# Kernel tuning notes

Measured on AMD Instinct MI355X. Metric: run time of the kernel, lower is better.

## Reference

```python
import jax, jax.numpy as jnp
import numpy as np

LARGE_NUMBER = 1e10
HIDDEN = 256
G = 32
NV = 64


def setup_inputs() -> dict:
    key = jax.random.key(0)
    k1, k2, k3, k4, k5, k6 = jax.random.split(key, 6)
    z = jax.random.normal(k1, (G * NV, HIDDEN), dtype=jnp.float32)
    mask = jax.random.randint(k2, (G * NV, 1), 0, 2).astype(jnp.float32)
    s = 1.0 / np.sqrt(HIDDEN)
    Wc = jax.random.uniform(k3, (HIDDEN, HIDDEN), jnp.float32, -s, s)
    bc = jax.random.uniform(k4, (HIDDEN,), jnp.float32, -s, s)
    Wy = jax.random.uniform(k5, (HIDDEN, HIDDEN), jnp.float32, -s, s)
    by = jax.random.uniform(k6, (HIDDEN,), jnp.float32, -s, s)
    return {"num_graphs": G, "nv": NV, "z": z, "mask": mask,
            "Wc": Wc, "bc": bc, "Wy": Wy, "by": by}


def reference(num_graphs, nv, z, mask, Wc, bc, Wy, by):
    H = z.shape[-1]
    z = z.reshape(num_graphs, nv, H)
    m = mask.reshape(num_graphs, nv, -1)          # [G, nv, 1]
    # Project ONCE per node (linearity makes this identical to projecting the
    # tiled [G,nv,nv,H] tensors as the torch code does).
    c = jnp.einsum('gnh,oh->gno', z, Wc) + bc     # lin_attention_c(z)
    y = jnp.einsum('gnh,oh->gno', z, Wy) + by     # lin_attention_y(z)
    # mask term: (m_i*L - L) + (m_j*L - L)
    mask_term = (m[:, :, None, :] + m[:, None, :, :]) * LARGE_NUMBER - 2.0 * LARGE_NUMBER
    # pairwise broadcast add + sigmoid: [G, nv, nv, H]
    s = jax.nn.sigmoid(c[:, :, None, :] + y[:, None, :, :] + mask_term)
    denom = jnp.sum(m, axis=1)[:, None, :]        # [G, 1, 1]
    out = jnp.sum(s, axis=2) / denom              # [G, nv, H]
    return out.reshape(-1, H)
```

## Files before the change

kernel.cpp:

```cpp
#include <hip/hip_runtime.h>

#define Gn    32
#define NVn   64
#define Hn    256
#define NROWS (Gn * NVn)

typedef __attribute__((ext_vector_type(8))) short  bf16x8;
typedef __attribute__((ext_vector_type(4))) float  f32x4;

__device__ inline unsigned short f2bf(float f) {
    unsigned int u = __builtin_bit_cast(unsigned int, f);
    return (unsigned short)((u + 0x7FFFu + ((u >> 16) & 1u)) >> 16);
}

__global__ __launch_bounds__(512) void gemm_exp_mfma(
    const float* __restrict__ z,
    const float* __restrict__ Wc, const float* __restrict__ bc,
    const float* __restrict__ Wy, const float* __restrict__ by,
    float* __restrict__ ws)
{
    const int n0    = blockIdx.x * 64;
    const int o0    = blockIdx.y * 64;
    const int which = blockIdx.z;
    const float* __restrict__ W    = which ? Wy : Wc;
    const float* __restrict__ bias = which ? by : bc;
    float* __restrict__ dst = ws + (size_t)which * NROWS * Hn;

    __shared__ unsigned short Za[64][40];
    __shared__ unsigned short Wb[64][40];

    const int t    = threadIdx.x;
    const int half = t >> 8;
    const int tt   = t & 255;
    const int srow = tt >> 2;
    const int sk   = (tt & 3) * 8;

    const float* src = half ? (W + (size_t)(o0 + srow) * Hn + sk)
                            : (z + (size_t)(n0 + srow) * Hn + sk);
    unsigned short* ldst = half ? &Wb[srow][sk] : &Za[srow][sk];

    const int wv = t >> 6;
    const int l  = t & 63;
    const int lm = l & 15;
    const int lq = l >> 4;
    const int ns = (wv & 3) * 16;
    const int oh = (wv >> 2) * 32;

    f32x4 acc[2] = {{0.f,0.f,0.f,0.f},{0.f,0.f,0.f,0.f}};

    float4 p0 = *(const float4*)(src);
    float4 p1 = *(const float4*)(src + 4);

    for (int kk = 0; kk < 8; ++kk) {
        bf16x8 v;
        v[0] = (short)f2bf(p0.x); v[1] = (short)f2bf(p0.y);
        v[2] = (short)f2bf(p0.z); v[3] = (short)f2bf(p0.w);
        v[4] = (short)f2bf(p1.x); v[5] = (short)f2bf(p1.y);
        v[6] = (short)f2bf(p1.z); v[7] = (short)f2bf(p1.w);
        *(bf16x8*)ldst = v;
        __syncthreads();

        if (kk < 7) {
            p0 = *(const float4*)(src + (kk + 1) * 32);
            p1 = *(const float4*)(src + (kk + 1) * 32 + 4);
        }

        const bf16x8 af = *(const bf16x8*)&Za[ns + lm][lq * 8];
        const bf16x8 b0 = *(const bf16x8*)&Wb[oh + lm][lq * 8];
        const bf16x8 b1 = *(const bf16x8*)&Wb[oh + 16 + lm][lq * 8];
        acc[0] = __builtin_amdgcn_mfma_f32_16x16x32_bf16(af, b0, acc[0], 0, 0, 0);
        acc[1] = __builtin_amdgcn_mfma_f32_16x16x32_bf16(af, b1, acc[1], 0, 0, 0);
        __syncthreads();
    }

#pragma unroll
    for (int ot = 0; ot < 2; ++ot) {
        const int o  = o0 + oh + ot * 16 + lm;
        const float bv = bias[o];
#pragma unroll
        for (int r = 0; r < 4; ++r) {
            const int n = n0 + ns + lq * 4 + r;
            dst[(size_t)n * Hn + o] = __expf(-(acc[ot][r] + bv));
        }
    }
}

__global__ __launch_bounds__(512) void pair_kernel(
    const float* __restrict__ mask,
    const float* __restrict__ ws,
    float* __restrict__ out)
{
    const float* __restrict__ ec = ws;
    const float* __restrict__ ey = ws + (size_t)NROWS * Hn;

    const int g  = blockIdx.x >> 3;
    const int i0 = (blockIdx.x & 7) * 8;
    const int t  = threadIdx.x;
    const int i  = i0 + (t >> 6);
    const int oc = (t & 63) * 4;

    __shared__ int act[64];
    __shared__ int cnt_s;

    if (t < 64) {
        const float m = mask[g * NVn + t];
        const unsigned long long b = __ballot(m != 0.f);
        const int below = __popcll(b & ((1ull << t) - 1ull));
        if (m != 0.f) act[below] = t;
        if (t == 0) cnt_s = (int)__popcll(b);
    }
    __syncthreads();
    const int cnt = cnt_s;

    const int row_i = g * NVn + i;
    float* po = out + (size_t)row_i * Hn + oc;

    const float mi = mask[row_i];
    if (mi == 0.f) {
        float4 zr; zr.x = zr.y = zr.z = zr.w = 0.f;
        *(float4*)po = zr;
        return;
    }

    const float4 ec4 = *(const float4*)(ec + (size_t)row_i * Hn + oc);
    const float* eyg = ey + (size_t)g * NVn * Hn + oc;

    float ax = 0.f, ay = 0.f, az = 0.f, aw = 0.f;
#pragma unroll 4
    for (int jj = 0; jj < cnt; ++jj) {
        const int j = act[jj];
        const float4 e4 = *(const float4*)(eyg + (size_t)j * Hn);
        ax += __builtin_amdgcn_rcpf(__builtin_fmaf(ec4.x, e4.x, 1.f));
        ay += __builtin_amdgcn_rcpf(__builtin_fmaf(ec4.y, e4.y, 1.f));
        az += __builtin_amdgcn_rcpf(__builtin_fmaf(ec4.z, e4.z, 1.f));
        aw += __builtin_amdgcn_rcpf(__builtin_fmaf(ec4.w, e4.w, 1.f));
    }

    const float s = 1.f / (float)cnt;
    float4 o4;
    o4.x = ax * s; o4.y = ay * s; o4.z = az * s; o4.w = aw * s;
    *(float4*)po = o4;
}

extern "C" void kernel_launch(void* const* d_in, const int* in_sizes, int n_in,
                              void* d_out, int out_size, void* d_ws, size_t ws_size,
                              hipStream_t stream) {
    const float* z    = (const float*)d_in[2];
    const float* mask = (const float*)d_in[3];
    const float* Wc   = (const float*)d_in[4];
    const float* bc   = (const float*)d_in[5];
    const float* Wy   = (const float*)d_in[6];
    const float* by   = (const float*)d_in[7];
    float* out = (float*)d_out;
    float* ws  = (float*)d_ws;

    dim3 gridA(NROWS / 64, Hn / 64, 2);
    gemm_exp_mfma<<<gridA, 512, 0, stream>>>(z, Wc, bc, Wy, by, ws);

    pair_kernel<<<Gn * 8, 512, 0, stream>>>(mask, ws, out);
}
```

Measured before the change: 81.33 us.

## Fuse projection GEMM and pairwise sigmoid sum into one per-graph kernel

The two kernels (MFMA projection with exp, then pairwise reduction) become a single kernel. Each block handles one graph and a 32-wide output slice, projects it with both weight matrices, and keeps the exp(-y) tile in shared memory for the pairwise sum. This removes the round trip of both projections through global memory and one kernel launch. In exchange, each block reloads and converts the whole 64x256 z tile for its graph, eight times per graph in total, and uses more shared memory per block. Block IDs are also remapped so blocks of the same graph are spread out.

```diff
diff --git a/kernel.cpp b/kernel.cpp
--- a/kernel.cpp
+++ b/kernel.cpp
@@ -3,7 +3,9 @@
 #define Gn    32
 #define NVn   64
 #define Hn    256
-#define NROWS (Gn * NVn)
+#define OT    32
+#define ZPAD  264
+#define EPAD  34
 
 typedef __attribute__((ext_vector_type(8))) short  bf16x8;
 typedef __attribute__((ext_vector_type(4))) float  f32x4;
@@ -13,133 +15,125 @@
     return (unsigned short)((u + 0x7FFFu + ((u >> 16) & 1u)) >> 16);
 }
 
-__global__ __launch_bounds__(512) void gemm_exp_mfma(
-    const float* __restrict__ z,
+__global__ __launch_bounds__(512) void fused_attn(
+    const float* __restrict__ z,  const float* __restrict__ mask,
     const float* __restrict__ Wc, const float* __restrict__ bc,
     const float* __restrict__ Wy, const float* __restrict__ by,
-    float* __restrict__ ws)
+    float* __restrict__ out)
 {
-    const int n0    = blockIdx.x * 64;
-    const int o0    = blockIdx.y * 64;
-    const int which = blockIdx.z;
-    const float* __restrict__ W    = which ? Wy : Wc;
-    const float* __restrict__ bias = which ? by : bc;
-    float* __restrict__ dst = ws + (size_t)which * NROWS * Hn;
+    const int phys = blockIdx.x;
+    const int lid  = (phys & 7) * 32 + (phys >> 3);
+    const int g    = lid >> 3;
+    const int o0   = (lid & 7) * OT;
 
-    __shared__ unsigned short Za[64][40];
-    __shared__ unsigned short Wb[64][40];
+    __shared__ __align__(16) unsigned short Zs[NVn][ZPAD];
+    __shared__ __align__(16) unsigned short Wsh[2 * OT][ZPAD];
+    __shared__ float eyL[NVn][EPAD];
+    __shared__ float mskL[NVn];
+    __shared__ int   act[NVn];
+    __shared__ int   cnt_s;
 
-    const int t    = threadIdx.x;
-    const int half = t >> 8;
-    const int tt   = t & 255;
-    const int srow = tt >> 2;
-    const int sk   = (tt & 3) * 8;
+    const int t = threadIdx.x;
 
-    const float* src = half ? (W + (size_t)(o0 + srow) * Hn + sk)
-                            : (z + (size_t)(n0 + srow) * Hn + sk);
-    unsigned short* ldst = half ? &Wb[srow][sk] : &Za[srow][sk];
+    if (t < 64) {
+        const float m = mask[g * NVn + t];
+        mskL[t] = m;
+        const unsigned long long b = __ballot(m != 0.f);
+        const int below = __popcll(b & ((1ull << t) - 1ull));
+        if (m != 0.f) act[below] = t;
+        if (t == 0) cnt_s = (int)__popcll(b);
+    }
+
+    const float* zg = z + (size_t)g * NVn * Hn;
+    float4 za[4], zb[4], wa[4], wb[4];
+#pragma unroll
+    for (int c = 0; c < 4; ++c) {
+        const int idx = t + c * 512;
+        const int row = idx >> 5;
+        const int k8  = (idx & 31) * 8;
+        const float* s = zg + (size_t)row * Hn + k8;
+        za[c] = *(const float4*)(s);
+        zb[c] = *(const float4*)(s + 4);
+    }
+#pragma unroll
+    for (int c = 0; c < 4; ++c) {
+        const int idx = t + c * 512;
+        const int row = idx >> 5;
+        const int k8  = (idx & 31) * 8;
+        const float* s = (row < OT) ? (Wc + (size_t)(o0 + row) * Hn + k8)
+                                    : (Wy + (size_t)(o0 + row - OT) * Hn + k8);
+        wa[c] = *(const float4*)(s);
+        wb[c] = *(const float4*)(s + 4);
+    }
+#pragma unroll
+    for (int c = 0; c < 4; ++c) {
+        const int idx = t + c * 512;
+        const int row = idx >> 5;
+        const int k8  = (idx & 31) * 8;
+        bf16x8 v;
+        v[0] = (short)f2bf(za[c].x); v[1] = (short)f2bf(za[c].y);
+        v[2] = (short)f2bf(za[c].z); v[3] = (short)f2bf(za[c].w);
+        v[4] = (short)f2bf(zb[c].x); v[5] = (short)f2bf(zb[c].y);
+        v[6] = (short)f2bf(zb[c].z); v[7] = (short)f2bf(zb[c].w);
+        *(bf16x8*)&Zs[row][k8] = v;
+        bf16x8 w;
+        w[0] = (short)f2bf(wa[c].x); w[1] = (short)f2bf(wa[c].y);
+        w[2] = (short)f2bf(wa[c].z); w[3] = (short)f2bf(wa[c].w);
+        w[4] = (short)f2bf(wb[c].x); w[5] = (short)f2bf(wb[c].y);
+        w[6] = (short)f2bf(wb[c].z); w[7] = (short)f2bf(wb[c].w);
+        *(bf16x8*)&Wsh[row][k8] = w;
+    }
+    __syncthreads();
 
     const int wv = t >> 6;
     const int l  = t & 63;
     const int lm = l & 15;
     const int lq = l >> 4;
     const int ns = (wv & 3) * 16;
-    const int oh = (wv >> 2) * 32;
+    const int oh = (wv >> 2) * 16;
 
-    f32x4 acc[2] = {{0.f,0.f,0.f,0.f},{0.f,0.f,0.f,0.f}};
-
-    float4 p0 = *(const float4*)(src);
-    float4 p1 = *(const float4*)(src + 4);
-
+    f32x4 accC = {0.f, 0.f, 0.f, 0.f};
+    f32x4 accY = {0.f, 0.f, 0.f, 0.f};
+#pragma unroll
     for (int kk = 0; kk < 8; ++kk) {
-        bf16x8 v;
-        v[0] = (short)f2bf(p0.x); v[1] = (short)f2bf(p0.y);
-        v[2] = (short)f2bf(p0.z); v[3] = (short)f2bf(p0.w);
-        v[4] = (short)f2bf(p1.x); v[5] = (short)f2bf(p1.y);
-        v[6] = (short)f2bf(p1.z); v[7] = (short)f2bf(p1.w);
-        *(bf16x8*)ldst = v;
-        __syncthreads();
-
-        if (kk < 7) {
-            p0 = *(const float4*)(src + (kk + 1) * 32);
-            p1 = *(const float4*)(src + (kk + 1) * 32 + 4);
-        }
-
-        const bf16x8 af = *(const bf16x8*)&Za[ns + lm][lq * 8];
-        const bf16x8 b0 = *(const bf16x8*)&Wb[oh + lm][lq * 8];
-        const bf16x8 b1 = *(const bf16x8*)&Wb[oh + 16 + lm][lq * 8];
-        acc[0] = __builtin_amdgcn_mfma_f32_16x16x32_bf16(af, b0, acc[0], 0, 0, 0);
-        acc[1] = __builtin_amdgcn_mfma_f32_16x16x32_bf16(af, b1, acc[1], 0, 0, 0);
-        __syncthreads();
+        const bf16x8 af  = *(const bf16x8*)&Zs[ns + lm][kk * 32 + lq * 8];
+        const bf16x8 bcf = *(const bf16x8*)&Wsh[oh + lm][kk * 32 + lq * 8];
+        const bf16x8 byf = *(const bf16x8*)&Wsh[OT + oh + lm][kk * 32 + lq * 8];
+        accC = __builtin_amdgcn_mfma_f32_16x16x32_bf16(af, bcf, accC, 0, 0, 0);
+        accY = __builtin_amdgcn_mfma_f32_16x16x32_bf16(af, byf, accY, 0, 0, 0);
     }
 
+    const int o_loc = oh + lm;
+    const int o     = o0 + o_loc;
+    const float bcv = bc[o];
+    const float byv = by[o];
+    float ecv[4];
 #pragma unroll
-    for (int ot = 0; ot < 2; ++ot) {
-        const int o  = o0 + oh + ot * 16 + lm;
-        const float bv = bias[o];
-#pragma unroll
-        for (int r = 0; r < 4; ++r) {
-            const int n = n0 + ns + lq * 4 + r;
-            dst[(size_t)n * Hn + o] = __expf(-(acc[ot][r] + bv));
-        }
-    }
-}
-
-__global__ __launch_bounds__(512) void pair_kernel(
-    const float* __restrict__ mask,
-    const float* __restrict__ ws,
-    float* __restrict__ out)
-{
-    const float* __restrict__ ec = ws;
-    const float* __restrict__ ey = ws + (size_t)NROWS * Hn;
-
-    const int g  = blockIdx.x >> 3;
-    const int i0 = (blockIdx.x & 7) * 8;
-    const int t  = threadIdx.x;
-    const int i  = i0 + (t >> 6);
-    const int oc = (t & 63) * 4;
-
-    __shared__ int act[64];
-    __shared__ int cnt_s;
-
-    if (t < 64) {
-        const float m = mask[g * NVn + t];
-        const unsigned long long b = __ballot(m != 0.f);
-        const int below = __popcll(b & ((1ull << t) - 1ull));
-        if (m != 0.f) act[below] = t;
-        if (t == 0) cnt_s = (int)__popcll(b);
+    for (int r = 0; r < 4; ++r) {
+        ecv[r] = __expf(-(accC[r] + bcv));
+        eyL[ns + lq * 4 + r][o_loc] = __expf(-(accY[r] + byv));
     }
     __syncthreads();
+
     const int cnt = cnt_s;
-
-    const int row_i = g * NVn + i;
-    float* po = out + (size_t)row_i * Hn + oc;
-
-    const float mi = mask[row_i];
-    if (mi == 0.f) {
-        float4 zr; zr.x = zr.y = zr.z = zr.w = 0.f;
-        *(float4*)po = zr;
-        return;
-    }
-
-    const float4 ec4 = *(const float4*)(ec + (size_t)row_i * Hn + oc);
-    const float* eyg = ey + (size_t)g * NVn * Hn + oc;
-
-    float ax = 0.f, ay = 0.f, az = 0.f, aw = 0.f;
+    float a0 = 0.f, a1 = 0.f, a2 = 0.f, a3 = 0.f;
 #pragma unroll 4
     for (int jj = 0; jj < cnt; ++jj) {
-        const int j = act[jj];
-        const float4 e4 = *(const float4*)(eyg + (size_t)j * Hn);
-        ax += __builtin_amdgcn_rcpf(__builtin_fmaf(ec4.x, e4.x, 1.f));
-        ay += __builtin_amdgcn_rcpf(__builtin_fmaf(ec4.y, e4.y, 1.f));
-        az += __builtin_amdgcn_rcpf(__builtin_fmaf(ec4.z, e4.z, 1.f));
-        aw += __builtin_amdgcn_rcpf(__builtin_fmaf(ec4.w, e4.w, 1.f));
+        const float ev = eyL[act[jj]][o_loc];
+        a0 += __builtin_amdgcn_rcpf(__builtin_fmaf(ecv[0], ev, 1.f));
+        a1 += __builtin_amdgcn_rcpf(__builtin_fmaf(ecv[1], ev, 1.f));
+        a2 += __builtin_amdgcn_rcpf(__builtin_fmaf(ecv[2], ev, 1.f));
+        a3 += __builtin_amdgcn_rcpf(__builtin_fmaf(ecv[3], ev, 1.f));
     }
-
-    const float s = 1.f / (float)cnt;
-    float4 o4;
-    o4.x = ax * s; o4.y = ay * s; o4.z = az * s; o4.w = aw * s;
-    *(float4*)po = o4;
+    const float inv = 1.f / (float)cnt;
+    float* og = out + (size_t)g * NVn * Hn + o;
+    const float s0 = a0 * inv, s1 = a1 * inv, s2 = a2 * inv, s3 = a3 * inv;
+    const float sv[4] = {s0, s1, s2, s3};
+#pragma unroll
+    for (int r = 0; r < 4; ++r) {
+        const int i = ns + lq * 4 + r;
+        og[(size_t)i * Hn] = (mskL[i] == 0.f) ? 0.f : sv[r];
+    }
 }
 
 extern "C" void kernel_launch(void* const* d_in, const int* in_sizes, int n_in,
@@ -152,10 +146,7 @@
     const float* Wy   = (const float*)d_in[6];
     const float* by   = (const float*)d_in[7];
     float* out = (float*)d_out;
-    float* ws  = (float*)d_ws;
+    (void)d_ws; (void)ws_size;
 
-    dim3 gridA(NROWS / 64, Hn / 64, 2);
-    gemm_exp_mfma<<<gridA, 512, 0, stream>>>(z, Wc, bc, Wy, by, ws);
-
-    pair_kernel<<<Gn * 8, 512, 0, stream>>>(mask, ws, out);
+    fused_attn<<<dim3(Gn * (Hn / OT)), 512, 0, stream>>>(z, mask, Wc, bc, Wy, by, out);
 }
```

Result: faster. 73.59 us (-9.5%).
